# Optimization experiments

Hardware: AMD Instinct MI355X
Metric: run time of the kernel (lower is better)

## Reference

```python
import jax, jax.numpy as jnp
import numpy as np
import math

B, SQ, SKV, D = 16, 1024, 1024, 256


def setup_inputs() -> dict:
    key = jax.random.key(0)
    kq, kk, kv, km = jax.random.split(key, 4)
    # Scale inputs down: the module applies exp() to raw QK^T logits, so dot
    # products must stay small to avoid overflow (std ~ 0.05^2*sqrt(D) ~ 0.04).
    scale = 0.05
    query = jax.random.normal(kq, (B, SQ, D), dtype=jnp.float32) * scale
    key_t = jax.random.normal(kk, (B, SKV, D), dtype=jnp.float32) * scale
    value = jax.random.normal(kv, (B, SKV, D), dtype=jnp.float32)
    mask = jax.random.randint(km, (B, SQ, SKV), 0, 2, dtype=jnp.int32)
    return {"query": query, "key": key_t, "value": value, "mask": mask}


def reference(query, key, value, mask):
    # scores = exp(Q K^T) / sqrt(d)  -- note: exp BEFORE scaling, as in source
    d = query.shape[-1]
    inv_sqrt_d = jnp.float32(1.0 / math.sqrt(d))
    scores = jnp.exp(jnp.einsum('bqd,bkd->bqk', query, key)) * inv_sqrt_d
    # masked_fill(mask == 0, -1e9)
    scores = jnp.where(mask == 0, jnp.float32(-1e9), scores)
    p_attn = jax.nn.softmax(scores, axis=-1)
    # dropout is identity in eval mode (deterministic reference)
    output = jnp.einsum('bqk,bkd->bqd', p_attn, value)
    # flatten=True path: sum over the query/sequence dim
    return output.sum(axis=1), p_attn
```

## Files before the change

kernel.cpp:

```cpp
#include <hip/hip_runtime.h>

#define NB   16
#define NSQ  1024
#define NSKV 1024
#define ND   256

typedef __bf16    bf16x8 __attribute__((ext_vector_type(8)));
typedef float     f32x4  __attribute__((ext_vector_type(4)));
typedef _Float16  f16x4  __attribute__((ext_vector_type(4)));

#define KST 264

__global__ __launch_bounds__(256) void prep_kernel(
    const float* __restrict__ K, __bf16* __restrict__ Kb,
    const int* __restrict__ mask, unsigned* __restrict__ mw,
    float* __restrict__ colsum, float* __restrict__ out0)
{
    const int bid = blockIdx.x;
    const int tid = threadIdx.x;
    if (bid < 2048) {
        const int i = bid * 256 + tid;
        const float4* s = (const float4*)K + (size_t)i * 2;
        float4 a = s[0], b = s[1];
        bf16x8 o;
        o[0] = (__bf16)a.x; o[1] = (__bf16)a.y; o[2] = (__bf16)a.z; o[3] = (__bf16)a.w;
        o[4] = (__bf16)b.x; o[5] = (__bf16)b.y; o[6] = (__bf16)b.z; o[7] = (__bf16)b.w;
        ((bf16x8*)Kb)[i] = o;
    } else if (bid < 2048 + 4096) {
        const int row = (bid - 2048) * 4 + (tid >> 6);
        const int l   = tid & 63;
        const int4* mrow = (const int4*)(mask + (size_t)row * NSKV) + l * 4;
        unsigned w = 0;
        #pragma unroll
        for (int v = 0; v < 4; ++v) {
            int4 mv = mrow[v];
            w |= (mv.x != 0 ? 1u : 0u) << (v * 4 + 0);
            w |= (mv.y != 0 ? 1u : 0u) << (v * 4 + 1);
            w |= (mv.z != 0 ? 1u : 0u) << (v * 4 + 2);
            w |= (mv.w != 0 ? 1u : 0u) << (v * 4 + 3);
        }
        const int m    = l & 15;
        const int base = l & 48;
        unsigned out = 0;
        #pragma unroll
        for (int c = 0; c < 16; ++c) {
            unsigned v = (unsigned)__shfl((int)w, base | c);
            out |= ((v >> m) & 1u) << c;
        }
        mw[(size_t)row * 64 + l] = out;
    } else if (bid < 2048 + 4096 + 64) {
        colsum[(bid - 6144) * 256 + tid] = 0.f;
    } else {
        out0[(bid - 6208) * 256 + tid] = 0.f;
    }
}

__global__ __launch_bounds__(256, 2) void attn_fused(
    const float* __restrict__ Q, const __bf16* __restrict__ Kb,
    const unsigned* __restrict__ mw, float* __restrict__ out_p,
    float* __restrict__ colsum)
{
    const int b    = blockIdx.x >> 6;
    const int qt   = blockIdx.x & 63;
    const int q0   = qt * 16;
    const int tid  = threadIdx.x;
    const int lane = tid & 63;
    const int h    = tid >> 6;
    const int m    = lane & 15;
    const int kg   = lane >> 4;

    __shared__ __attribute__((aligned(16))) __bf16 kbuf[4][2][16 * KST];
    __shared__ float Zs[4][16];
    __shared__ float invZs[16];

    bf16x8 afrag[8];
    {
        const float* qbase = Q + ((size_t)(b * NSQ + q0 + m)) * ND;
        #pragma unroll
        for (int dc = 0; dc < 8; ++dc) {
            const float* p4 = qbase + dc * 32 + kg * 8;
            float4 x = *(const float4*)(p4);
            float4 y = *(const float4*)(p4 + 4);
            bf16x8 a;
            a[0] = (__bf16)x.x; a[1] = (__bf16)x.y; a[2] = (__bf16)x.z; a[3] = (__bf16)x.w;
            a[4] = (__bf16)y.x; a[5] = (__bf16)y.y; a[6] = (__bf16)y.z; a[7] = (__bf16)y.w;
            afrag[dc] = a;
        }
    }

    unsigned mword[4];
    #pragma unroll
    for (int i = 0; i < 4; ++i)
        mword[i] = mw[(size_t)(b * NSQ + q0 + kg * 4 + i) * 64 + h * 16 + m];

    const __bf16* kq   = Kb + ((size_t)(b * NSKV + h * 256)) * ND;
    const int     gcol = (lane & 31) * 8;
    const int     grow = lane >> 5;
    __bf16* buf0 = &kbuf[h][0][0];
    __bf16* buf1 = &kbuf[h][1][0];

    float  zacc[4] = {0.f, 0.f, 0.f, 0.f};
    f16x4  ebuf[16];
    bf16x8 ga[8], gb[8];

    #define LDCHUNK(g, c) { \
        const __bf16* _p = kq + (size_t)(c) * 16 * ND + gcol; \
        _Pragma("unroll") \
        for (int r = 0; r < 8; ++r) \
            (g)[r] = *(const bf16x8*)(_p + (size_t)(2 * r + grow) * ND); }

    #define STCHUNK(g, buf) { \
        _Pragma("unroll") \
        for (int r = 0; r < 8; ++r) \
            *(bf16x8*)((buf) + (2 * r + grow) * KST + gcol) = (g)[r]; }

    #define COMPUTE(buf, c) { \
        f32x4 acc = {0.f, 0.f, 0.f, 0.f}; \
        _Pragma("unroll") \
        for (int dc = 0; dc < 8; ++dc) { \
            bf16x8 bfr = *(const bf16x8*)((buf) + m * KST + dc * 32 + kg * 8); \
            acc = __builtin_amdgcn_mfma_f32_16x16x32_bf16(afrag[dc], bfr, acc, 0, 0, 0); \
        } \
        _Pragma("unroll") \
        for (int i = 0; i < 4; ++i) { \
            float e = ((mword[i] >> (c)) & 1u) ? __expf(__expf(acc[i]) * 0.0625f) : 0.f; \
            zacc[i] += e; \
            ebuf[c][i] = (_Float16)e; \
        } }

    LDCHUNK(ga, 0);
    LDCHUNK(gb, 1);
    STCHUNK(ga, buf0);

    #pragma unroll
    for (int cc = 0; cc < 16; cc += 2) {
        if (cc + 2 < 16) LDCHUNK(ga, cc + 2);
        COMPUTE(buf0, cc);
        STCHUNK(gb, buf1);
        if (cc + 3 < 16) LDCHUNK(gb, cc + 3);
        COMPUTE(buf1, cc + 1);
        if (cc + 2 < 16) STCHUNK(ga, buf0);
    }

    _Float16* myE = (_Float16*)&kbuf[h][0][0];
    #pragma unroll
    for (int c = 0; c < 16; ++c)
        #pragma unroll
        for (int i = 0; i < 4; ++i)
            myE[(kg * 4 + i) * KST + c * 16 + m] = ebuf[c][i];

    #pragma unroll
    for (int i = 0; i < 4; ++i) {
        float z = zacc[i];
        z += __shfl_xor(z, 1);
        z += __shfl_xor(z, 2);
        z += __shfl_xor(z, 4);
        z += __shfl_xor(z, 8);
        if (m == 0) Zs[h][kg * 4 + i] = z;
    }
    __syncthreads();
    if (tid < 16)
        invZs[tid] = 1.0f / (Zs[0][tid] + Zs[1][tid] + Zs[2][tid] + Zs[3][tid]);
    __syncthreads();

    float csum[4] = {0.f, 0.f, 0.f, 0.f};
    float* prow = out_p + (size_t)(b * NSQ + q0) * NSKV + h * 256 + lane * 4;
    #pragma unroll
    for (int s = 0; s < 16; ++s) {
        f16x4 ev = *(const f16x4*)&myE[s * KST + lane * 4];
        const float iz = invZs[s];
        float4 pv;
        pv.x = (float)ev[0] * iz; pv.y = (float)ev[1] * iz;
        pv.z = (float)ev[2] * iz; pv.w = (float)ev[3] * iz;
        *(float4*)(prow + (size_t)s * NSKV) = pv;
        csum[0] += pv.x; csum[1] += pv.y; csum[2] += pv.z; csum[3] += pv.w;
    }
    #pragma unroll
    for (int j = 0; j < 4; ++j)
        atomicAdd(&colsum[b * NSKV + h * 256 + lane * 4 + j], csum[j]);

    #undef LDCHUNK
    #undef STCHUNK
    #undef COMPUTE
}

__global__ __launch_bounds__(256) void attn_out_kernel(
    const float* __restrict__ colsum, const float* __restrict__ V,
    float* __restrict__ out)
{
    const int b  = blockIdx.x >> 6;
    const int ks = (blockIdx.x & 63) << 4;
    const int d  = threadIdx.x;
    float acc = 0.f;
    #pragma unroll
    for (int k = 0; k < 16; ++k) {
        acc += colsum[b * NSKV + ks + k] * V[((size_t)(b * NSKV + ks + k)) * ND + d];
    }
    atomicAdd(&out[b * ND + d], acc);
}

extern "C" void kernel_launch(void* const* d_in, const int* in_sizes, int n_in,
                              void* d_out, int out_size, void* d_ws, size_t ws_size,
                              hipStream_t stream)
{
    (void)in_sizes; (void)n_in; (void)out_size; (void)ws_size;
    const float* Q    = (const float*)d_in[0];
    const float* K    = (const float*)d_in[1];
    const float* V    = (const float*)d_in[2];
    const int*   mask = (const int*)d_in[3];

    float* out0 = (float*)d_out;
    float* p    = out0 + NB * ND;

    float*    colsum = (float*)d_ws;
    __bf16*   Kb     = (__bf16*)((char*)d_ws + (64 << 10));
    unsigned* mwbits = (unsigned*)((char*)d_ws + (64 << 10) + (size_t)NB * NSKV * ND * 2);

    prep_kernel<<<6224, 256, 0, stream>>>(K, Kb, mask, mwbits, colsum, out0);
    attn_fused<<<NB * 64, 256, 0, stream>>>(Q, Kb, mwbits, p, colsum);
    attn_out_kernel<<<NB * 64, 256, 0, stream>>>(colsum, V, out0);
}
```

Before: 200.8 us.

## Pre-swizzle K into MFMA fragment layout and load B fragments directly from global

The prep kernel now writes bf16 K in the exact per-lane MFMA B-fragment order, so the attention kernel loads fragments straight from global memory into registers. This removes the LDS staging buffers and the store/load round trip, and exp values are written to a smaller LDS parking area during compute instead of held in registers. The lower LDS and register use allows raising launch bounds to 4 blocks per CU. In exchange, each wave issues more global loads per chunk and depends on the cache to hide their latency, since there is no longer any cross-lane sharing through LDS.

```diff
diff --git a/kernel.cpp b/kernel.cpp
--- a/kernel.cpp
+++ b/kernel.cpp
@@ -9,23 +9,30 @@
 typedef float     f32x4  __attribute__((ext_vector_type(4)));
 typedef _Float16  f16x4  __attribute__((ext_vector_type(4)));
 
-#define KST 264
+#define EST 268
 
 __global__ __launch_bounds__(256) void prep_kernel(
-    const float* __restrict__ K, __bf16* __restrict__ Kb,
+    const float* __restrict__ K, __bf16* __restrict__ Kbf,
     const int* __restrict__ mask, unsigned* __restrict__ mw,
     float* __restrict__ colsum, float* __restrict__ out0)
 {
     const int bid = blockIdx.x;
     const int tid = threadIdx.x;
     if (bid < 2048) {
-        const int i = bid * 256 + tid;
-        const float4* s = (const float4*)K + (size_t)i * 2;
-        float4 a = s[0], b = s[1];
+        const int i    = bid * 256 + tid;
+        const int lane = i & 63;
+        const int m    = lane & 15;
+        const int kg   = lane >> 4;
+        const int dc   = (i >> 6) & 7;
+        const int kvb  = (i >> 9) & 63;
+        const int b    = i >> 15;
+        const float* s = K + ((size_t)(b * NSKV + kvb * 16 + m)) * ND + dc * 32 + kg * 8;
+        float4 a = *(const float4*)s;
+        float4 c = *(const float4*)(s + 4);
         bf16x8 o;
         o[0] = (__bf16)a.x; o[1] = (__bf16)a.y; o[2] = (__bf16)a.z; o[3] = (__bf16)a.w;
-        o[4] = (__bf16)b.x; o[5] = (__bf16)b.y; o[6] = (__bf16)b.z; o[7] = (__bf16)b.w;
-        ((bf16x8*)Kb)[i] = o;
+        o[4] = (__bf16)c.x; o[5] = (__bf16)c.y; o[6] = (__bf16)c.z; o[7] = (__bf16)c.w;
+        ((bf16x8*)Kbf)[i] = o;
     } else if (bid < 2048 + 4096) {
         const int row = (bid - 2048) * 4 + (tid >> 6);
         const int l   = tid & 63;
@@ -55,8 +62,8 @@
     }
 }
 
-__global__ __launch_bounds__(256, 2) void attn_fused(
-    const float* __restrict__ Q, const __bf16* __restrict__ Kb,
+__global__ __launch_bounds__(256, 4) void attn_fused(
+    const float* __restrict__ Q, const __bf16* __restrict__ Kbf,
     const unsigned* __restrict__ mw, float* __restrict__ out_p,
     float* __restrict__ colsum)
 {
@@ -69,9 +76,11 @@
     const int m    = lane & 15;
     const int kg   = lane >> 4;
 
-    __shared__ __attribute__((aligned(16))) __bf16 kbuf[4][2][16 * KST];
+    __shared__ __attribute__((aligned(16))) _Float16 epark[4][16 * EST];
     __shared__ float Zs[4][16];
     __shared__ float invZs[16];
+
+    _Float16* myE = &epark[h][0];
 
     bf16x8 afrag[8];
     {
@@ -93,61 +102,37 @@
     for (int i = 0; i < 4; ++i)
         mword[i] = mw[(size_t)(b * NSQ + q0 + kg * 4 + i) * 64 + h * 16 + m];
 
-    const __bf16* kq   = Kb + ((size_t)(b * NSKV + h * 256)) * ND;
-    const int     gcol = (lane & 31) * 8;
-    const int     grow = lane >> 5;
-    __bf16* buf0 = &kbuf[h][0][0];
-    __bf16* buf1 = &kbuf[h][1][0];
-
-    float  zacc[4] = {0.f, 0.f, 0.f, 0.f};
-    f16x4  ebuf[16];
-    bf16x8 ga[8], gb[8];
-
-    #define LDCHUNK(g, c) { \
-        const __bf16* _p = kq + (size_t)(c) * 16 * ND + gcol; \
+    const bf16x8* kf = (const bf16x8*)Kbf + ((size_t)(b * 64 + h * 16) * 8) * 64 + lane;
+
+    float zacc[4] = {0.f, 0.f, 0.f, 0.f};
+    bf16x8 fA[8], fB[8];
+
+    #define LDFRAG(g, c) { \
         _Pragma("unroll") \
-        for (int r = 0; r < 8; ++r) \
-            (g)[r] = *(const bf16x8*)(_p + (size_t)(2 * r + grow) * ND); }
-
-    #define STCHUNK(g, buf) { \
-        _Pragma("unroll") \
-        for (int r = 0; r < 8; ++r) \
-            *(bf16x8*)((buf) + (2 * r + grow) * KST + gcol) = (g)[r]; }
-
-    #define COMPUTE(buf, c) { \
+        for (int dc = 0; dc < 8; ++dc) \
+            (g)[dc] = kf[((c) * 8 + dc) * 64]; }
+
+    #define COMPUTE(g, c) { \
         f32x4 acc = {0.f, 0.f, 0.f, 0.f}; \
         _Pragma("unroll") \
-        for (int dc = 0; dc < 8; ++dc) { \
-            bf16x8 bfr = *(const bf16x8*)((buf) + m * KST + dc * 32 + kg * 8); \
-            acc = __builtin_amdgcn_mfma_f32_16x16x32_bf16(afrag[dc], bfr, acc, 0, 0, 0); \
-        } \
+        for (int dc = 0; dc < 8; ++dc) \
+            acc = __builtin_amdgcn_mfma_f32_16x16x32_bf16(afrag[dc], (g)[dc], acc, 0, 0, 0); \
         _Pragma("unroll") \
         for (int i = 0; i < 4; ++i) { \
             float e = ((mword[i] >> (c)) & 1u) ? __expf(__expf(acc[i]) * 0.0625f) : 0.f; \
             zacc[i] += e; \
-            ebuf[c][i] = (_Float16)e; \
+            myE[(kg * 4 + i) * EST + (c) * 16 + m] = (_Float16)e; \
         } }
 
-    LDCHUNK(ga, 0);
-    LDCHUNK(gb, 1);
-    STCHUNK(ga, buf0);
+    LDFRAG(fA, 0);
 
     #pragma unroll
     for (int cc = 0; cc < 16; cc += 2) {
-        if (cc + 2 < 16) LDCHUNK(ga, cc + 2);
-        COMPUTE(buf0, cc);
-        STCHUNK(gb, buf1);
-        if (cc + 3 < 16) LDCHUNK(gb, cc + 3);
-        COMPUTE(buf1, cc + 1);
-        if (cc + 2 < 16) STCHUNK(ga, buf0);
-    }
-
-    _Float16* myE = (_Float16*)&kbuf[h][0][0];
-    #pragma unroll
-    for (int c = 0; c < 16; ++c)
-        #pragma unroll
-        for (int i = 0; i < 4; ++i)
-            myE[(kg * 4 + i) * KST + c * 16 + m] = ebuf[c][i];
+        LDFRAG(fB, cc + 1);
+        COMPUTE(fA, cc);
+        if (cc + 2 < 16) LDFRAG(fA, cc + 2);
+        COMPUTE(fB, cc + 1);
+    }
 
     #pragma unroll
     for (int i = 0; i < 4; ++i) {
@@ -167,7 +152,7 @@
     float* prow = out_p + (size_t)(b * NSQ + q0) * NSKV + h * 256 + lane * 4;
     #pragma unroll
     for (int s = 0; s < 16; ++s) {
-        f16x4 ev = *(const f16x4*)&myE[s * KST + lane * 4];
+        f16x4 ev = *(const f16x4*)&myE[s * EST + lane * 4];
         const float iz = invZs[s];
         float4 pv;
         pv.x = (float)ev[0] * iz; pv.y = (float)ev[1] * iz;
@@ -179,8 +164,7 @@
     for (int j = 0; j < 4; ++j)
         atomicAdd(&colsum[b * NSKV + h * 256 + lane * 4 + j], csum[j]);
 
-    #undef LDCHUNK
-    #undef STCHUNK
+    #undef LDFRAG
     #undef COMPUTE
 }
 
@@ -213,10 +197,10 @@
     float* p    = out0 + NB * ND;
 
     float*    colsum = (float*)d_ws;
-    __bf16*   Kb     = (__bf16*)((char*)d_ws + (64 << 10));
+    __bf16*   Kbf    = (__bf16*)((char*)d_ws + (64 << 10));
     unsigned* mwbits = (unsigned*)((char*)d_ws + (64 << 10) + (size_t)NB * NSKV * ND * 2);
 
-    prep_kernel<<<6224, 256, 0, stream>>>(K, Kb, mask, mwbits, colsum, out0);
-    attn_fused<<<NB * 64, 256, 0, stream>>>(Q, Kb, mwbits, p, colsum);
+    prep_kernel<<<6224, 256, 0, stream>>>(K, Kbf, mask, mwbits, colsum, out0);
+    attn_fused<<<NB * 64, 256, 0, stream>>>(Q, Kbf, mwbits, p, colsum);
     attn_out_kernel<<<NB * 64, 256, 0, stream>>>(colsum, V, out0);
 }
```

After: 204.3 us. Within noise of the previous version (+1.7%).
